# Kernel tuning notes

Hardware: AMD Instinct MI355X
Metric: run time of the kernel (lower is better)

## Reference

```python
import jax, jax.numpy as jnp
import numpy as np

N = 10000        # nodes
E = 120000       # edges
IN_W = 6         # in_width
KER_IN = 6       # edge-attr dim
WN = 32          # width_node
WK = 256         # width_kernel
DEPTH = 4


def setup_inputs() -> dict:
    key = jax.random.key(0)
    ks = jax.random.split(key, 16)

    def w(k, shape, fan_in):
        return (jax.random.normal(k, shape, jnp.float32) / np.sqrt(fan_in)).astype(jnp.float32)

    return {
        "x": jax.random.normal(ks[0], (N, IN_W), jnp.float32),
        "edge_index": jax.random.randint(ks[1], (2, E), 0, N, jnp.int64 if jax.config.jax_enable_x64 else jnp.int32),
        "edge_attr": jax.random.uniform(ks[2], (E, KER_IN), jnp.float32),
        # fc1: in_width -> width_node
        "fc1_w": w(ks[3], (IN_W, WN), IN_W), "fc1_b": jnp.zeros((WN,), jnp.float32),
        # DenseNet kernel: ker_in -> WK//2 -> WK -> WN*WN (ReLU between, none after last)
        "k1_w": w(ks[4], (KER_IN, WK // 2), KER_IN), "k1_b": jnp.zeros((WK // 2,), jnp.float32),
        "k2_w": w(ks[5], (WK // 2, WK), WK // 2),    "k2_b": jnp.zeros((WK,), jnp.float32),
        "k3_w": w(ks[6], (WK, WN * WN), WK),         "k3_b": jnp.zeros((WN * WN,), jnp.float32),
        # NNConv root weight + bias
        "root_w": w(ks[7], (WN, WN), WN), "conv_b": jnp.zeros((WN,), jnp.float32),
        # fc2: WN -> 128, fc3: 128 -> 1
        "fc2_w": w(ks[8], (WN, 128), WN), "fc2_b": jnp.zeros((128,), jnp.float32),
        "fc3_w": w(ks[9], (128, 1), 128), "fc3_b": jnp.zeros((1,), jnp.float32),
    }


def reference(x, edge_index, edge_attr,
              fc1_w, fc1_b, k1_w, k1_b, k2_w, k2_b, k3_w, k3_b,
              root_w, conv_b, fc2_w, fc2_b, fc3_w, fc3_b):
    src, dst = edge_index[0], edge_index[1]

    # Edge-conditioned weight matrices via DenseNet kernel MLP (same edge_attr
    # every layer -> identical weights each depth step; compute once).
    h_e = jax.nn.relu(edge_attr @ k1_w + k1_b)
    h_e = jax.nn.relu(h_e @ k2_w + k2_b)
    w_e = (h_e @ k3_w + k3_b).reshape(E, WN, WN)   # [E, in, out]

    # scatter-mean denominator (in-degree, clamped to 1)
    cnt = jax.ops.segment_sum(jnp.ones((E,), jnp.float32), dst, num_segments=N)
    denom = jnp.maximum(cnt, 1.0)[:, None]

    h = x @ fc1_w + fc1_b                          # [N, WN]
    for d in range(DEPTH):
        msg = jnp.einsum('ei,eio->eo', h[src], w_e)          # per-edge matvec
        aggr = jax.ops.segment_sum(msg, dst, num_segments=N) / denom
        h = aggr + h @ root_w + conv_b             # NNConv: aggr + root + bias
        if d != DEPTH - 1:
            h = jax.nn.relu(h)

    h = jax.nn.relu(h @ fc2_w + fc2_b)
    return h @ fc3_w + fc3_b                       # [N, 1]
```

## Files before the change

kernel.cpp:

```cpp
#include <hip/hip_runtime.h>
#include <hip/hip_bf16.h>

#define NN 10000
#define EE 120000
#define E_PAD 120064
#define NT64 1876

#define H1S 136
#define H2S 264

typedef __bf16 bf16_t;
typedef __bf16 bf16x8 __attribute__((ext_vector_type(8)));
typedef float f32x4 __attribute__((ext_vector_type(4)));

static __device__ __forceinline__ int clampi(int v) {
    return v < 0 ? 0 : (v >= NN ? NN - 1 : v);
}

__global__ __launch_bounds__(256) void detect_f32(const unsigned short* __restrict__ ea_raw,
                                                  int* __restrict__ flag) {
    int t = blockIdx.x * 256 + threadIdx.x;
    if (ea_raw[t] & 0x8000) atomicOr(flag, 1);
}

#define N_FLT 16
struct CvtArgs {
    const void* src[N_FLT];
    float* dst;
    int offs[N_FLT];
    int n[N_FLT];
    int tot;
};

__global__ __launch_bounds__(256) void cvt_flat(CvtArgs a, const int* __restrict__ isf32) {
    int i = blockIdx.x * 256 + threadIdx.x;
    if (i >= a.tot) return;
    int t = 0;
#pragma unroll
    for (int k = 1; k < N_FLT; ++k) if (i >= a.offs[k]) t = k;
    int il = i - a.offs[t];
    float v;
    if (*isf32) v = ((const float*)a.src[t])[il];
    else        v = (float)((const bf16_t*)a.src[t])[il];
    if (!isfinite(v)) v = 0.f;
    a.dst[i] = v;
}

__global__ __launch_bounds__(256) void detect_idx(const int* __restrict__ ei,
                                                  int* __restrict__ flag) {
    int t = blockIdx.x * 256 + threadIdx.x;
    if (ei[2 * t + 1] != 0) atomicOr(flag, 1);
}

__global__ __launch_bounds__(256) void repack_idx(const int* __restrict__ ei,
                                                  const int* __restrict__ flag,
                                                  int* __restrict__ s,
                                                  int* __restrict__ d,
                                                  int* __restrict__ cnti) {
    int e = blockIdx.x * 256 + threadIdx.x;
    if (e >= EE) return;
    int sv, dv;
    if (*flag == 0) {
        sv = clampi(ei[2 * e]);
        dv = clampi(ei[2 * (EE + e)]);
    } else {
        sv = clampi(ei[e]);
        dv = clampi(ei[EE + e]);
    }
    s[e] = sv;
    d[e] = dv;
    atomicAdd(&cnti[dv], 1);
}

__global__ __launch_bounds__(256) void scan_kernel(const int* __restrict__ cnti,
                                                   int* __restrict__ row_off,
                                                   int* __restrict__ pos) {
    __shared__ int part[256];
    const int t = threadIdx.x;
    const int CH = (NN + 255) / 256;
    int s = 0;
    for (int i = 0; i < CH; ++i) {
        int idx = t * CH + i;
        if (idx < NN) s += cnti[idx];
    }
    part[t] = s;
    __syncthreads();
    for (int off = 1; off < 256; off <<= 1) {
        int tmp = (t >= off) ? part[t - off] : 0;
        __syncthreads();
        part[t] += tmp;
        __syncthreads();
    }
    int run = part[t] - s;
    for (int i = 0; i < CH; ++i) {
        int idx = t * CH + i;
        if (idx < NN) {
            row_off[idx] = run;
            pos[idx] = run;
            run += cnti[idx];
        }
    }
    if (t == 255) row_off[NN] = run;
}

__global__ __launch_bounds__(256) void scatter_rank(const int* __restrict__ dst,
                                                    const int* __restrict__ src,
                                                    int* __restrict__ pos,
                                                    int* __restrict__ rank,
                                                    int* __restrict__ src_s) {
    int e = blockIdx.x * 256 + threadIdx.x;
    if (e >= E_PAD) return;
    if (e >= EE) { rank[e] = e; return; }
    int p = atomicAdd(&pos[dst[e]], 1);
    rank[e] = p;
    src_s[p] = src[e];
}


__global__ __launch_bounds__(256) void transpose_bt(const float* __restrict__ B,
                                                    bf16_t* __restrict__ Bt, int K, int N,
                                                    int permute) {
    int idx = blockIdx.x * 256 + threadIdx.x;
    if (idx >= K * N) return;
    int n = idx / K, k = idx - n * K;
    int c = permute ? (((n & 31) << 5) | (n >> 5)) : n;
    Bt[idx] = (bf16_t)B[k * N + c];
}

__global__ __launch_bounds__(256) void permute_bias(const float* __restrict__ b,
                                                    float* __restrict__ bp) {
    int n = blockIdx.x * 256 + threadIdx.x;
    bp[n] = b[((n & 31) << 5) | (n >> 5)];
}

__global__ __launch_bounds__(256) void h0_kernel(const float* __restrict__ x,
                                                 const float* __restrict__ w,
                                                 const float* __restrict__ b,
                                                 float* __restrict__ h) {
    int gid = blockIdx.x * 256 + threadIdx.x;
    int n = gid >> 5, o = gid & 31;
    float acc = b[o];
#pragma unroll
    for (int j = 0; j < 6; ++j) acc += x[n * 6 + j] * w[j * 32 + o];
    h[gid] = acc;
}

__global__ __launch_bounds__(256) void fused_prep(const float* __restrict__ ea,
                                                  const float* __restrict__ k1w,
                                                  const float* __restrict__ k1b,
                                                  const bf16_t* __restrict__ k2t,
                                                  const float* __restrict__ k2b,
                                                  const bf16_t* __restrict__ k3t,
                                                  const float* __restrict__ k3bp,
                                                  bf16_t* __restrict__ we,
                                                  const int* __restrict__ rank,
                                                  int tile0, int perm) {
    __shared__ bf16_t h1_s[64 * H1S];
    __shared__ bf16_t h2_s[64 * H2S];
    float* ea_s  = (float*)h2_s;
    float* k1w_s = ea_s + 64 * 6;
    float* k1b_s = k1w_s + 768;

    const int t = threadIdx.x;
    const int tile = tile0 + blockIdx.x;
    const int e0 = tile * 64;

    for (int i = t; i < 384; i += 256) {
        int r = i / 6, j = i - r * 6;
        int e = e0 + r;
        ea_s[i] = (e < EE) ? ea[(size_t)e * 6 + j] : 0.f;
    }
    for (int i = t; i < 768; i += 256) k1w_s[i] = k1w[i];
    if (t < 128) k1b_s[t] = k1b[t];
    __syncthreads();

    {
        const int o = t & 127, rh = t >> 7;
        for (int r = rh * 32; r < rh * 32 + 32; ++r) {
            float acc = k1b_s[o];
#pragma unroll
            for (int j = 0; j < 6; ++j) acc += ea_s[r * 6 + j] * k1w_s[j * 128 + o];
            h1_s[r * H1S + o] = (bf16_t)fmaxf(acc, 0.f);
        }
    }
    __syncthreads();

    const int lane = t & 63;
    const int w = t >> 6;
    const int nr16 = lane & 15;
    const int koff = (lane >> 4) * 8;
    const int rbase = (lane >> 4) * 4;

    {
        f32x4 acc[4][4];
#pragma unroll
        for (int i = 0; i < 4; ++i)
#pragma unroll
            for (int j = 0; j < 4; ++j) acc[i][j] = f32x4{0.f, 0.f, 0.f, 0.f};
#pragma unroll
        for (int ks = 0; ks < 4; ++ks) {
            const int k0 = ks * 32;
            bf16x8 af[4], bfr[4];
#pragma unroll
            for (int i = 0; i < 4; ++i)
                af[i] = *(const bf16x8*)&h1_s[(nr16 + i * 16) * H1S + k0 + koff];
#pragma unroll
            for (int j = 0; j < 4; ++j)
                bfr[j] = *(const bf16x8*)&k2t[(w * 64 + j * 16 + nr16) * 128 + k0 + koff];
#pragma unroll
            for (int i = 0; i < 4; ++i)
#pragma unroll
                for (int j = 0; j < 4; ++j)
                    acc[i][j] = __builtin_amdgcn_mfma_f32_16x16x32_bf16(af[i], bfr[j], acc[i][j], 0, 0, 0);
        }
#pragma unroll
        for (int i = 0; i < 4; ++i) {
#pragma unroll
            for (int j = 0; j < 4; ++j) {
                int col = w * 64 + j * 16 + nr16;
                float bv = k2b[col];
#pragma unroll
                for (int r = 0; r < 4; ++r) {
                    int row = i * 16 + rbase + r;
                    h2_s[row * H2S + col] = (bf16_t)fmaxf(acc[i][j][r] + bv, 0.f);
                }
            }
        }
    }
    __syncthreads();

#pragma unroll 1
    for (int nt = 0; nt < 4; ++nt) {
        const int c0 = nt * 256 + w * 64;
        f32x4 acc[4][4];
#pragma unroll
        for (int i = 0; i < 4; ++i)
#pragma unroll
            for (int j = 0; j < 4; ++j) acc[i][j] = f32x4{0.f, 0.f, 0.f, 0.f};
#pragma unroll 1
        for (int ks = 0; ks < 8; ++ks) {
            const int k0 = ks * 32;
            bf16x8 af[4], bfr[4];
#pragma unroll
            for (int i = 0; i < 4; ++i)
                af[i] = *(const bf16x8*)&h2_s[(nr16 + i * 16) * H2S + k0 + koff];
#pragma unroll
            for (int j = 0; j < 4; ++j)
                bfr[j] = *(const bf16x8*)&k3t[(size_t)(c0 + j * 16 + nr16) * 256 + k0 + koff];
#pragma unroll
            for (int i = 0; i < 4; ++i)
#pragma unroll
                for (int j = 0; j < 4; ++j)
                    acc[i][j] = __builtin_amdgcn_mfma_f32_16x16x32_bf16(af[i], bfr[j], acc[i][j], 0, 0, 0);
        }
#pragma unroll
        for (int i = 0; i < 4; ++i) {
#pragma unroll
            for (int r = 0; r < 4; ++r) {
                int lr = i * 16 + rbase + r;
                long er = (long)e0 + lr;
                long crow = perm ? (long)rank[er] : (long)blockIdx.x * 64 + lr;
#pragma unroll
                for (int j = 0; j < 4; ++j) {
                    int col = c0 + j * 16 + nr16;
                    we[crow * 1024 + col] = (bf16_t)(acc[i][j][r] + k3bp[col]);
                }
            }
        }
    }
}

__global__ __launch_bounds__(256) void gather_stream(const float* __restrict__ h,
                                                     const bf16_t* __restrict__ wt,
                                                     const int* __restrict__ src_s,
                                                     const int* __restrict__ row_off,
                                                     const float* __restrict__ rw,
                                                     const float* __restrict__ cb,
                                                     float* __restrict__ hout,
                                                     int relu, int rev) {
    __shared__ float rws[1024];
    for (int i = threadIdx.x; i < 1024; i += 256) rws[i] = rw[i];
    __syncthreads();
    const int wv = threadIdx.x >> 6, lane = threadIdx.x & 63;
    const int nb = rev ? ((int)gridDim.x - 1 - blockIdx.x) : blockIdx.x;
    const int n = nb * 4 + wv;
    if (n >= NN) return;
    const int o = lane >> 1, half = lane & 1;

    const int b0 = row_off[n], b1 = row_off[n + 1];
    float acc = 0.f;
    if (b0 < b1) {
        int s = src_s[b0];
        const float4* hp = (const float4*)(h + (size_t)s * 32 + half * 16);
        float4 ha = hp[0], hb = hp[1], hcv = hp[2], hd = hp[3];
        const bf16x8* wp = (const bf16x8*)(wt + (size_t)b0 * 1024 + lane * 16);
        bf16x8 w0 = wp[0], w1 = wp[1];
        for (int k = b0; k + 1 < b1; ++k) {
            int s2 = src_s[k + 1];
            const float4* hp2 = (const float4*)(h + (size_t)s2 * 32 + half * 16);
            float4 na = hp2[0], nb2 = hp2[1], nc = hp2[2], nd = hp2[3];
            const bf16x8* wp2 = (const bf16x8*)(wt + (size_t)(k + 1) * 1024 + lane * 16);
            bf16x8 nw0 = wp2[0], nw1 = wp2[1];
            acc += ha.x * (float)w0[0] + ha.y * (float)w0[1]
                 + ha.z * (float)w0[2] + ha.w * (float)w0[3]
                 + hb.x * (float)w0[4] + hb.y * (float)w0[5]
                 + hb.z * (float)w0[6] + hb.w * (float)w0[7]
                 + hcv.x * (float)w1[0] + hcv.y * (float)w1[1]
                 + hcv.z * (float)w1[2] + hcv.w * (float)w1[3]
                 + hd.x * (float)w1[4] + hd.y * (float)w1[5]
                 + hd.z * (float)w1[6] + hd.w * (float)w1[7];
            ha = na; hb = nb2; hcv = nc; hd = nd; w0 = nw0; w1 = nw1;
        }
        acc += ha.x * (float)w0[0] + ha.y * (float)w0[1]
             + ha.z * (float)w0[2] + ha.w * (float)w0[3]
             + hb.x * (float)w0[4] + hb.y * (float)w0[5]
             + hb.z * (float)w0[6] + hb.w * (float)w0[7]
             + hcv.x * (float)w1[0] + hcv.y * (float)w1[1]
             + hcv.z * (float)w1[2] + hcv.w * (float)w1[3]
             + hd.x * (float)w1[4] + hd.y * (float)w1[5]
             + hd.z * (float)w1[6] + hd.w * (float)w1[7];
    }

    float rp = 0.f;
    const float4* hn = (const float4*)(h + (size_t)n * 32 + half * 16);
    float4 a = hn[0], b = hn[1], c = hn[2], dd = hn[3];
    const float* rwb = &rws[half * 16 * 32 + o];
    rp += a.x * rwb[0]   + a.y * rwb[32]  + a.z * rwb[64]  + a.w * rwb[96];
    rp += b.x * rwb[128] + b.y * rwb[160] + b.z * rwb[192] + b.w * rwb[224];
    rp += c.x * rwb[256] + c.y * rwb[288] + c.z * rwb[320] + c.w * rwb[352];
    rp += dd.x * rwb[384] + dd.y * rwb[416] + dd.z * rwb[448] + dd.w * rwb[480];

    acc += __shfl_xor(acc, 1, 64);
    rp  += __shfl_xor(rp, 1, 64);
    if (half == 0) {
        float den = fmaxf((float)(b1 - b0), 1.f);
        float v = acc / den + rp + cb[o];
        if (relu) v = fmaxf(v, 0.f);
        hout[(size_t)n * 32 + o] = v;
    }
}

__global__ __launch_bounds__(256) void edge_scatter(const float* __restrict__ h,
                                                    const bf16_t* __restrict__ wt,
                                                    const int* __restrict__ src,
                                                    const int* __restrict__ dst,
                                                    float* __restrict__ aggr,
                                                    int e0, int e1) {
    int wv = threadIdx.x >> 6, lane = threadIdx.x & 63;
    int e = e0 + blockIdx.x * 4 + wv;
    if (e >= e1) return;
    int s = src[e], d = dst[e];
    int o = lane & 31, ihalf = lane >> 5;
    const float4* hp = (const float4*)(h + (size_t)s * 32 + ihalf * 16);
    float4 ha = hp[0], hb = hp[1], hcv = hp[2], hd = hp[3];
    const bf16x8* wp = (const bf16x8*)(wt + (size_t)(e - e0) * 1024 + o * 32 + ihalf * 16);
    bf16x8 w0 = wp[0], w1 = wp[1];
    float acc = ha.x * (float)w0[0] + ha.y * (float)w0[1]
              + ha.z * (float)w0[2] + ha.w * (float)w0[3]
              + hb.x * (float)w0[4] + hb.y * (float)w0[5]
              + hb.z * (float)w0[6] + hb.w * (float)w0[7]
              + hcv.x * (float)w1[0] + hcv.y * (float)w1[1]
              + hcv.z * (float)w1[2] + hcv.w * (float)w1[3]
              + hd.x * (float)w1[4] + hd.y * (float)w1[5]
              + hd.z * (float)w1[6] + hd.w * (float)w1[7];
    acc += __shfl_xor(acc, 32, 64);
    if (ihalf == 0) atomicAdd(&aggr[(size_t)d * 32 + o], acc);
}

__global__ __launch_bounds__(256) void node_update(const float* __restrict__ hin,
                                                   const float* __restrict__ aggr,
                                                   const int* __restrict__ cnti,
                                                   const float* __restrict__ rw,
                                                   const float* __restrict__ cb,
                                                   float* __restrict__ hout, int relu) {
    __shared__ float rws[32 * 32];
    for (int i = threadIdx.x; i < 1024; i += 256) rws[i] = rw[i];
    __syncthreads();
    int gid = blockIdx.x * 256 + threadIdx.x;
    int n = gid >> 5, o = gid & 31;
    float den = fmaxf((float)cnti[n], 1.f);
    float acc = aggr[gid] / den + cb[o];
    const float* hrow = hin + (size_t)n * 32;
#pragma unroll
    for (int j = 0; j < 32; ++j) acc += hrow[j] * rws[j * 32 + o];
    if (relu) acc = fmaxf(acc, 0.f);
    hout[gid] = acc;
}

__global__ __launch_bounds__(256) void head_kernel(const float* __restrict__ h,
                                                   const float* __restrict__ w2,
                                                   const float* __restrict__ b2,
                                                   const float* __restrict__ w3,
                                                   const float* __restrict__ b3,
                                                   void* __restrict__ out,
                                                   const int* __restrict__ isf32) {
    int wave = threadIdx.x >> 6, lane = threadIdx.x & 63;
    int n = blockIdx.x * 4 + wave;
    if (n >= NN) return;
    const float* hrow = h + (size_t)n * 32;
    float hr[32];
#pragma unroll
    for (int j = 0; j < 32; ++j) hr[j] = hrow[j];
    int o0 = lane * 2, o1 = lane * 2 + 1;
    float v0 = b2[o0], v1 = b2[o1];
#pragma unroll
    for (int j = 0; j < 32; ++j) {
        float hj = hr[j];
        v0 += hj * w2[j * 128 + o0];
        v1 += hj * w2[j * 128 + o1];
    }
    float y = fmaxf(v0, 0.f) * w3[o0] + fmaxf(v1, 0.f) * w3[o1];
#pragma unroll
    for (int m = 1; m < 64; m <<= 1) y += __shfl_xor(y, m, 64);
    if (lane == 0) {
        float r = y + b3[0];
        if (*isf32) ((float*)out)[n] = r;
        else        ((bf16_t*)out)[n] = (bf16_t)r;
    }
}


extern "C" void kernel_launch(void* const* d_in, const int* in_sizes, int n_in,
                              void* d_out, int out_size, void* d_ws, size_t ws_size,
                              hipStream_t stream) {
    const int* ei = (const int*)d_in[1];

    char* ws = (char*)d_ws;
    size_t off = 0;
    auto alignup = [](size_t b) { return (b + 255) & ~(size_t)255; };
    auto alloc = [&](size_t bytes) {
        char* p = ws + off;
        off += alignup(bytes);
        return (void*)p;
    };
    float*  h_a   = (float*)alloc((size_t)NN * 32 * 4);
    float*  h_b   = (float*)alloc((size_t)NN * 32 * 4);
    int*    cnti  = (int*)alloc((size_t)NN * 4);
    int*    rowo  = (int*)alloc((size_t)(NN + 1) * 4);
    int*    pos   = (int*)alloc((size_t)NN * 4);
    int*    f32fl = (int*)alloc(256);
    int*    idxfl = (int*)alloc(256);
    int*    srcb  = (int*)alloc((size_t)EE * 4);
    int*    dstb  = (int*)alloc((size_t)EE * 4);
    int*    rankb = (int*)alloc((size_t)E_PAD * 4);
    int*    src_s = (int*)alloc((size_t)E_PAD * 4);
    bf16_t* k2t   = (bf16_t*)alloc(256 * 128 * 2);
    bf16_t* k3t   = (bf16_t*)alloc(1024 * 256 * 2);
    float*  k3bp  = (float*)alloc(1024 * 4);

    static const int fidx[N_FLT] = {0, 2, 3, 4, 5, 6, 7, 8, 9, 10, 11, 12, 13, 14, 15, 16};
    static const int fn[N_FLT]   = {NN * 6, EE * 6, 192, 32, 768, 128, 32768, 256,
                                    262144, 1024, 1024, 32, 4096, 128, 128, 1};
    int foffs[N_FLT];
    int tot = 0;
    for (int i = 0; i < N_FLT; ++i) { foffs[i] = tot; tot += fn[i]; }
    float* canon = (float*)alloc((size_t)tot * 4);
    const float* c_x    = canon + foffs[0];
    const float* c_ea   = canon + foffs[1];
    const float* c_fc1w = canon + foffs[2];
    const float* c_fc1b = canon + foffs[3];
    const float* c_k1w  = canon + foffs[4];
    const float* c_k1b  = canon + foffs[5];
    const float* c_k2w  = canon + foffs[6];
    const float* c_k2b  = canon + foffs[7];
    const float* c_k3w  = canon + foffs[8];
    const float* c_k3b  = canon + foffs[9];
    const float* c_rw   = canon + foffs[10];
    const float* c_cb   = canon + foffs[11];
    const float* c_fc2w = canon + foffs[12];
    const float* c_fc2b = canon + foffs[13];
    const float* c_fc3w = canon + foffs[14];
    const float* c_fc3b = canon + foffs[15];
    size_t fixed_end = off;

    const size_t sz_we = (size_t)E_PAD * 1024 * 2;
    int mode, T;
    if (ws_size >= fixed_end + sz_we + 1024) { mode = 1; T = NT64; }
    else {
        mode = 0;
        size_t per_tile = (size_t)64 * 1024 * 2;
        size_t extra = alignup((size_t)NN * 32 * 4);
        size_t avail = ws_size > fixed_end + extra + 4096
                     ? ws_size - fixed_end - extra - 4096 : per_tile;
        long t = (long)(avail / per_tile);
        if (t > NT64) t = NT64;
        if (t < 1) t = 1;
        T = (int)t;
    }
    bf16_t* w_e = nullptr;
    float* aggr = nullptr;
    if (mode == 1) {
        w_e = (bf16_t*)alloc(sz_we);
    } else {
        aggr = (float*)alloc((size_t)NN * 32 * 4);
        w_e  = (bf16_t*)alloc((size_t)T * 64 * 1024 * 2);
    }

    hipMemsetAsync(cnti, 0, (size_t)NN * 4, stream);
    hipMemsetAsync(f32fl, 0, 256, stream);
    hipMemsetAsync(idxfl, 0, 256, stream);

    detect_f32<<<32, 256, 0, stream>>>((const unsigned short*)d_in[2], f32fl);

    CvtArgs ca;
    for (int i = 0; i < N_FLT; ++i) {
        ca.src[i] = d_in[fidx[i]];
        ca.offs[i] = foffs[i];
        ca.n[i] = fn[i];
    }
    ca.dst = canon;
    ca.tot = tot;
    cvt_flat<<<(tot + 255) / 256, 256, 0, stream>>>(ca, f32fl);

    detect_idx<<<16, 256, 0, stream>>>(ei, idxfl);
    repack_idx<<<(EE + 255) / 256, 256, 0, stream>>>(ei, idxfl, srcb, dstb, cnti);
    scan_kernel<<<1, 256, 0, stream>>>(cnti, rowo, pos);
    scatter_rank<<<(E_PAD + 255) / 256, 256, 0, stream>>>(dstb, srcb, pos, rankb, src_s);

    transpose_bt<<<(128 * 256 + 255) / 256, 256, 0, stream>>>(c_k2w, k2t, 128, 256, 0);
    transpose_bt<<<(256 * 1024 + 255) / 256, 256, 0, stream>>>(c_k3w, k3t, 256, 1024, 1);
    permute_bias<<<4, 256, 0, stream>>>(c_k3b, k3bp);
    h0_kernel<<<NN * 32 / 256, 256, 0, stream>>>(c_x, c_fc1w, c_fc1b, h_a);

    float* hc = h_a;
    float* hn = h_b;
    if (mode == 1) {
        fused_prep<<<NT64, 256, 0, stream>>>(c_ea, c_k1w, c_k1b, k2t, c_k2b,
                                             k3t, k3bp, w_e, rankb, 0, 1);
        for (int d = 0; d < 4; ++d) {
            gather_stream<<<(NN + 3) / 4, 256, 0, stream>>>(hc, w_e, src_s, rowo,
                                                            c_rw, c_cb, hn,
                                                            (d < 3) ? 1 : 0, d & 1);
            float* tmp = hc; hc = hn; hn = tmp;
        }
    } else {
        for (int d = 0; d < 4; ++d) {
            hipMemsetAsync(aggr, 0, (size_t)NN * 32 * 4, stream);
            for (int t0 = 0; t0 < NT64; t0 += T) {
                int tl = (t0 + T <= NT64) ? T : (NT64 - t0);
                fused_prep<<<tl, 256, 0, stream>>>(c_ea, c_k1w, c_k1b, k2t, c_k2b,
                                                   k3t, k3bp, w_e, rankb, t0, 0);
                int e0 = t0 * 64;
                int e1 = e0 + tl * 64; if (e1 > EE) e1 = EE;
                if (e1 > e0)
                    edge_scatter<<<(e1 - e0 + 3) / 4, 256, 0, stream>>>(hc, w_e, srcb, dstb,
                                                                        aggr, e0, e1);
            }
            node_update<<<NN * 32 / 256, 256, 0, stream>>>(hc, aggr, cnti, c_rw, c_cb, hn,
                                                           (d < 3) ? 1 : 0);
            float* tmp = hc; hc = hn; hn = tmp;
        }
    }

    head_kernel<<<(NN + 3) / 4, 256, 0, stream>>>(hc, c_fc2w, c_fc2b, c_fc3w, c_fc3b,
                                                  d_out, f32fl);
}
```

Measured before the change: 540.3 us.

## Merge small prep kernels, coalesce memsets, prefetch B fragments in fused_prep

Merges the two detection kernels into one and folds the transpose, bias-permute and h0 kernels into a single misc_prep launch. The three memsets become one over a contiguous region, cutting launch overhead. In fused_prep, B-operand fragments are software-prefetched one k-step ahead, the rank lookups and bias loads are hoisted out of the output loops, and a launch-bounds occupancy hint of 3 is added. The prefetch and the occupancy hint add register pressure, which could cause spills.

```diff
diff --git a/kernel.cpp b/kernel.cpp
--- a/kernel.cpp
+++ b/kernel.cpp
@@ -17,10 +17,13 @@
     return v < 0 ? 0 : (v >= NN ? NN - 1 : v);
 }
 
-__global__ __launch_bounds__(256) void detect_f32(const unsigned short* __restrict__ ea_raw,
-                                                  int* __restrict__ flag) {
+__global__ __launch_bounds__(256) void detect_all(const unsigned short* __restrict__ ea_raw,
+                                                  const int* __restrict__ ei,
+                                                  int* __restrict__ f32fl,
+                                                  int* __restrict__ idxfl) {
     int t = blockIdx.x * 256 + threadIdx.x;
-    if (ea_raw[t] & 0x8000) atomicOr(flag, 1);
+    if (ea_raw[t] & 0x8000) atomicOr(f32fl, 1);
+    if (t < 4096 && ei[2 * t + 1] != 0) atomicOr(idxfl, 1);
 }
 
 #define N_FLT 16
@@ -44,12 +47,6 @@
     else        v = (float)((const bf16_t*)a.src[t])[il];
     if (!isfinite(v)) v = 0.f;
     a.dst[i] = v;
-}
-
-__global__ __launch_bounds__(256) void detect_idx(const int* __restrict__ ei,
-                                                  int* __restrict__ flag) {
-    int t = blockIdx.x * 256 + threadIdx.x;
-    if (ei[2 * t + 1] != 0) atomicOr(flag, 1);
 }
 
 __global__ __launch_bounds__(256) void repack_idx(const int* __restrict__ ei,
@@ -116,45 +113,48 @@
     src_s[p] = src[e];
 }
 
-
-__global__ __launch_bounds__(256) void transpose_bt(const float* __restrict__ B,
-                                                    bf16_t* __restrict__ Bt, int K, int N,
-                                                    int permute) {
-    int idx = blockIdx.x * 256 + threadIdx.x;
-    if (idx >= K * N) return;
-    int n = idx / K, k = idx - n * K;
-    int c = permute ? (((n & 31) << 5) | (n >> 5)) : n;
-    Bt[idx] = (bf16_t)B[k * N + c];
-}
-
-__global__ __launch_bounds__(256) void permute_bias(const float* __restrict__ b,
-                                                    float* __restrict__ bp) {
-    int n = blockIdx.x * 256 + threadIdx.x;
-    bp[n] = b[((n & 31) << 5) | (n >> 5)];
-}
-
-__global__ __launch_bounds__(256) void h0_kernel(const float* __restrict__ x,
-                                                 const float* __restrict__ w,
-                                                 const float* __restrict__ b,
-                                                 float* __restrict__ h) {
-    int gid = blockIdx.x * 256 + threadIdx.x;
-    int n = gid >> 5, o = gid & 31;
-    float acc = b[o];
-#pragma unroll
-    for (int j = 0; j < 6; ++j) acc += x[n * 6 + j] * w[j * 32 + o];
-    h[gid] = acc;
-}
-
-__global__ __launch_bounds__(256) void fused_prep(const float* __restrict__ ea,
-                                                  const float* __restrict__ k1w,
-                                                  const float* __restrict__ k1b,
-                                                  const bf16_t* __restrict__ k2t,
-                                                  const float* __restrict__ k2b,
-                                                  const bf16_t* __restrict__ k3t,
-                                                  const float* __restrict__ k3bp,
-                                                  bf16_t* __restrict__ we,
-                                                  const int* __restrict__ rank,
-                                                  int tile0, int perm) {
+__global__ __launch_bounds__(256) void misc_prep(const float* __restrict__ k2w,
+                                                 bf16_t* __restrict__ k2t,
+                                                 const float* __restrict__ k3w,
+                                                 bf16_t* __restrict__ k3t,
+                                                 const float* __restrict__ k3b,
+                                                 float* __restrict__ k3bp,
+                                                 const float* __restrict__ x,
+                                                 const float* __restrict__ fc1w,
+                                                 const float* __restrict__ fc1b,
+                                                 float* __restrict__ h0) {
+    int i = blockIdx.x * 256 + threadIdx.x;
+    if (i < 32768) {
+        int n = i >> 7, k = i & 127;
+        k2t[i] = (bf16_t)k2w[k * 256 + n];
+    } else if (i < 294912) {
+        int idx = i - 32768;
+        int n = idx >> 8, k = idx & 255;
+        int c = ((n & 31) << 5) | (n >> 5);
+        k3t[idx] = (bf16_t)k3w[k * 1024 + c];
+    } else if (i < 295936) {
+        int n = i - 294912;
+        k3bp[n] = k3b[((n & 31) << 5) | (n >> 5)];
+    } else if (i < 615936) {
+        int gid = i - 295936;
+        int n = gid >> 5, o = gid & 31;
+        float acc = fc1b[o];
+#pragma unroll
+        for (int j = 0; j < 6; ++j) acc += x[n * 6 + j] * fc1w[j * 32 + o];
+        h0[gid] = acc;
+    }
+}
+
+__global__ __launch_bounds__(256, 3) void fused_prep(const float* __restrict__ ea,
+                                                     const float* __restrict__ k1w,
+                                                     const float* __restrict__ k1b,
+                                                     const bf16_t* __restrict__ k2t,
+                                                     const float* __restrict__ k2b,
+                                                     const bf16_t* __restrict__ k3t,
+                                                     const float* __restrict__ k3bp,
+                                                     bf16_t* __restrict__ we,
+                                                     const int* __restrict__ rank,
+                                                     int tile0, int perm) {
     __shared__ bf16_t h1_s[64 * H1S];
     __shared__ bf16_t h2_s[64 * H2S];
     float* ea_s  = (float*)h2_s;
@@ -197,21 +197,29 @@
         for (int i = 0; i < 4; ++i)
 #pragma unroll
             for (int j = 0; j < 4; ++j) acc[i][j] = f32x4{0.f, 0.f, 0.f, 0.f};
-#pragma unroll
+        bf16x8 bcur[4], bnxt[4];
+#pragma unroll
+        for (int j = 0; j < 4; ++j)
+            bcur[j] = *(const bf16x8*)&k2t[(w * 64 + j * 16 + nr16) * 128 + koff];
+#pragma unroll 1
         for (int ks = 0; ks < 4; ++ks) {
             const int k0 = ks * 32;
-            bf16x8 af[4], bfr[4];
+            if (ks < 3) {
+#pragma unroll
+                for (int j = 0; j < 4; ++j)
+                    bnxt[j] = *(const bf16x8*)&k2t[(w * 64 + j * 16 + nr16) * 128 + k0 + 32 + koff];
+            }
+            bf16x8 af[4];
 #pragma unroll
             for (int i = 0; i < 4; ++i)
                 af[i] = *(const bf16x8*)&h1_s[(nr16 + i * 16) * H1S + k0 + koff];
 #pragma unroll
-            for (int j = 0; j < 4; ++j)
-                bfr[j] = *(const bf16x8*)&k2t[(w * 64 + j * 16 + nr16) * 128 + k0 + koff];
-#pragma unroll
             for (int i = 0; i < 4; ++i)
 #pragma unroll
                 for (int j = 0; j < 4; ++j)
-                    acc[i][j] = __builtin_amdgcn_mfma_f32_16x16x32_bf16(af[i], bfr[j], acc[i][j], 0, 0, 0);
+                    acc[i][j] = __builtin_amdgcn_mfma_f32_16x16x32_bf16(af[i], bcur[j], acc[i][j], 0, 0, 0);
+#pragma unroll
+            for (int j = 0; j < 4; ++j) bcur[j] = bnxt[j];
         }
 #pragma unroll
         for (int i = 0; i < 4; ++i) {
@@ -229,41 +237,59 @@
     }
     __syncthreads();
 
+    int crow[4][4];
+#pragma unroll
+    for (int i = 0; i < 4; ++i)
+#pragma unroll
+        for (int r = 0; r < 4; ++r) {
+            int lr = i * 16 + rbase + r;
+            crow[i][r] = perm ? rank[e0 + lr] : (int)blockIdx.x * 64 + lr;
+        }
+
 #pragma unroll 1
     for (int nt = 0; nt < 4; ++nt) {
         const int c0 = nt * 256 + w * 64;
+        float bj[4];
+#pragma unroll
+        for (int j = 0; j < 4; ++j) bj[j] = k3bp[c0 + j * 16 + nr16];
         f32x4 acc[4][4];
 #pragma unroll
         for (int i = 0; i < 4; ++i)
 #pragma unroll
             for (int j = 0; j < 4; ++j) acc[i][j] = f32x4{0.f, 0.f, 0.f, 0.f};
+        bf16x8 bcur[4], bnxt[4];
+#pragma unroll
+        for (int j = 0; j < 4; ++j)
+            bcur[j] = *(const bf16x8*)&k3t[(size_t)(c0 + j * 16 + nr16) * 256 + koff];
 #pragma unroll 1
         for (int ks = 0; ks < 8; ++ks) {
             const int k0 = ks * 32;
-            bf16x8 af[4], bfr[4];
+            if (ks < 7) {
+#pragma unroll
+                for (int j = 0; j < 4; ++j)
+                    bnxt[j] = *(const bf16x8*)&k3t[(size_t)(c0 + j * 16 + nr16) * 256 + k0 + 32 + koff];
+            }
+            bf16x8 af[4];
 #pragma unroll
             for (int i = 0; i < 4; ++i)
                 af[i] = *(const bf16x8*)&h2_s[(nr16 + i * 16) * H2S + k0 + koff];
 #pragma unroll
-            for (int j = 0; j < 4; ++j)
-                bfr[j] = *(const bf16x8*)&k3t[(size_t)(c0 + j * 16 + nr16) * 256 + k0 + koff];
-#pragma unroll
             for (int i = 0; i < 4; ++i)
 #pragma unroll
                 for (int j = 0; j < 4; ++j)
-                    acc[i][j] = __builtin_amdgcn_mfma_f32_16x16x32_bf16(af[i], bfr[j], acc[i][j], 0, 0, 0);
+                    acc[i][j] = __builtin_amdgcn_mfma_f32_16x16x32_bf16(af[i], bcur[j], acc[i][j], 0, 0, 0);
+#pragma unroll
+            for (int j = 0; j < 4; ++j) bcur[j] = bnxt[j];
         }
 #pragma unroll
         for (int i = 0; i < 4; ++i) {
 #pragma unroll
             for (int r = 0; r < 4; ++r) {
-                int lr = i * 16 + rbase + r;
-                long er = (long)e0 + lr;
-                long crow = perm ? (long)rank[er] : (long)blockIdx.x * 64 + lr;
+                long cr = crow[i][r];
 #pragma unroll
                 for (int j = 0; j < 4; ++j) {
                     int col = c0 + j * 16 + nr16;
-                    we[crow * 1024 + col] = (bf16_t)(acc[i][j][r] + k3bp[col]);
+                    we[cr * 1024 + col] = (bf16_t)(acc[i][j][r] + bj[j]);
                 }
             }
         }
@@ -435,11 +461,13 @@
     };
     float*  h_a   = (float*)alloc((size_t)NN * 32 * 4);
     float*  h_b   = (float*)alloc((size_t)NN * 32 * 4);
+    char*   zbase = ws + off;
     int*    cnti  = (int*)alloc((size_t)NN * 4);
+    int*    f32fl = (int*)alloc(256);
+    int*    idxfl = (int*)alloc(256);
+    size_t  zlen  = (ws + off) - zbase;
     int*    rowo  = (int*)alloc((size_t)(NN + 1) * 4);
     int*    pos   = (int*)alloc((size_t)NN * 4);
-    int*    f32fl = (int*)alloc(256);
-    int*    idxfl = (int*)alloc(256);
     int*    srcb  = (int*)alloc((size_t)EE * 4);
     int*    dstb  = (int*)alloc((size_t)EE * 4);
     int*    rankb = (int*)alloc((size_t)E_PAD * 4);
@@ -496,11 +524,9 @@
         w_e  = (bf16_t*)alloc((size_t)T * 64 * 1024 * 2);
     }
 
-    hipMemsetAsync(cnti, 0, (size_t)NN * 4, stream);
-    hipMemsetAsync(f32fl, 0, 256, stream);
-    hipMemsetAsync(idxfl, 0, 256, stream);
-
-    detect_f32<<<32, 256, 0, stream>>>((const unsigned short*)d_in[2], f32fl);
+    hipMemsetAsync(zbase, 0, zlen, stream);
+
+    detect_all<<<32, 256, 0, stream>>>((const unsigned short*)d_in[2], ei, f32fl, idxfl);
 
     CvtArgs ca;
     for (int i = 0; i < N_FLT; ++i) {
@@ -512,15 +538,13 @@
     ca.tot = tot;
     cvt_flat<<<(tot + 255) / 256, 256, 0, stream>>>(ca, f32fl);
 
-    detect_idx<<<16, 256, 0, stream>>>(ei, idxfl);
     repack_idx<<<(EE + 255) / 256, 256, 0, stream>>>(ei, idxfl, srcb, dstb, cnti);
     scan_kernel<<<1, 256, 0, stream>>>(cnti, rowo, pos);
     scatter_rank<<<(E_PAD + 255) / 256, 256, 0, stream>>>(dstb, srcb, pos, rankb, src_s);
 
-    transpose_bt<<<(128 * 256 + 255) / 256, 256, 0, stream>>>(c_k2w, k2t, 128, 256, 0);
-    transpose_bt<<<(256 * 1024 + 255) / 256, 256, 0, stream>>>(c_k3w, k3t, 256, 1024, 1);
-    permute_bias<<<4, 256, 0, stream>>>(c_k3b, k3bp);
-    h0_kernel<<<NN * 32 / 256, 256, 0, stream>>>(c_x, c_fc1w, c_fc1b, h_a);
+    misc_prep<<<(615936 + 255) / 256, 256, 0, stream>>>(c_k2w, k2t, c_k3w, k3t,
+                                                        c_k3b, k3bp, c_x, c_fc1w,
+                                                        c_fc1b, h_a);
 
     float* hc = h_a;
     float* hn = h_b;
```

New measurement: 492.7 us. 8.8% less time.
